# Optimization experiments

Hardware: AMD Instinct MI355X
Metric: run time of the kernel (lower is better)

The kernel has to match this reference:

```python
import jax, jax.numpy as jnp
import numpy as np

N = 8192
D_IN = 256
D_HID = 256
D_OUT = 256


def setup_inputs() -> dict:
    key = jax.random.key(0)
    k_x, k_a, k_q, k_k, k_v = jax.random.split(key, 5)
    X = jax.random.normal(k_x, (N, D_IN), dtype=jnp.float32)
    # binary adjacency, zero diagonal (module adds self-loops via +eye)
    A = jax.random.randint(k_a, (N, N), 0, 2, dtype=jnp.int32)
    A = A * (1 - jnp.eye(N, dtype=jnp.int32))
    # parameters: randn / 10, as in the torch __init__
    Wq = jax.random.normal(k_q, (D_IN, D_HID), dtype=jnp.float32) / 10.0
    Wk = jax.random.normal(k_k, (D_IN, D_HID), dtype=jnp.float32) / 10.0
    Wv = jax.random.normal(k_v, (D_IN, D_OUT), dtype=jnp.float32) / 10.0
    return {"X": X, "A": A, "Wq": Wq, "Wk": Wk, "Wv": Wv}


def reference(X, A, Wq, Wk, Wv):
    n = A.shape[0]
    Af = A.astype(X.dtype) + jnp.eye(n, dtype=X.dtype)  # add self-loops
    Q = X @ Wq  # [N, H]
    K = X @ Wk  # [N, H]
    V = X @ Wv  # [N, O]
    S = Q @ K.T  # [N, N]
    # torch: nan_to_num(-inf*(1-A), nan=0) -> 0 where A==1, finite-min where A==0
    mask = jnp.nan_to_num(-jnp.inf * (1.0 - Af), nan=0.0)
    P = jax.nn.softmax(S + mask, axis=1)
    return P @ V  # [N, O]
```

## Files before the change

kernel.cpp:

```cpp
#include <hip/hip_runtime.h>
#include <stdint.h>


typedef _Float16 f16;
typedef unsigned short u16;
typedef __attribute__((ext_vector_type(8))) _Float16 f16x8;
typedef __attribute__((ext_vector_type(4))) _Float16 f16x4;
typedef __attribute__((ext_vector_type(4))) float f32x4;

#define NN 8192
#define DD 256
#define BR 128
#define BC 64
#define CCH 4
#define COLS (NN / CCH)
#define NIT (COLS / BC)

#define MFMA(a, b, c) __builtin_amdgcn_mfma_f32_16x16x32_f16((a), (b), (c), 0, 0, 0)

__device__ __forceinline__ void gl2lds16(const void* g, void* l) {
    __builtin_amdgcn_global_load_lds(
        (const __attribute__((address_space(1))) unsigned int*)g,
        (__attribute__((address_space(3))) unsigned int*)l, 16, 0, 0);
}

__device__ __forceinline__ u16 f16bits(f16 h) {
    union { f16 h; u16 u; } c;
    c.h = h;
    return c.u;
}

__global__ void splitX_kernel(const float4* __restrict__ X, f16x4* __restrict__ Xh,
                              f16x4* __restrict__ Xl) {
    const int i = blockIdx.x * blockDim.x + threadIdx.x;
    const float4 v = X[i];
    const f16 h0 = (f16)v.x, h1 = (f16)v.y, h2 = (f16)v.z, h3 = (f16)v.w;
    f16x4 H = {h0, h1, h2, h3};
    f16x4 L = {(f16)(v.x - (float)h0), (f16)(v.y - (float)h1), (f16)(v.z - (float)h2),
               (f16)(v.w - (float)h3)};
    Xh[i] = H;
    Xl[i] = L;
}

__global__ void splitW_kernel(const float* __restrict__ Wq, const float* __restrict__ Wk,
                              const float* __restrict__ Wv, f16* __restrict__ WtH,
                              f16* __restrict__ WtL) {
    const int i = blockIdx.x * blockDim.x + threadIdx.x;
    const int mat = i >> 16;
    const int k = (i >> 8) & 255;
    const int n = i & 255;
    const float* W = (mat == 0) ? Wq : ((mat == 1) ? Wk : Wv);
    const float v = W[k * 256 + n];
    const f16 h = (f16)v;
    const size_t o = (size_t)(mat * 256 + n) * 256 + k;
    WtH[o] = h;
    WtL[o] = (f16)(v - (float)h);
}

__global__ __launch_bounds__(256, 2) void qkv_kernel(
    const f16* __restrict__ Xh, const f16* __restrict__ Xl,
    const f16* __restrict__ WtH, const f16* __restrict__ WtL,
    f16* __restrict__ Qh, f16* __restrict__ Ql,
    f16* __restrict__ Kh, f16* __restrict__ Vt) {
    __shared__ f16 Wh[64 * 256];
    __shared__ f16 Wl[64 * 256];
    const int lane = threadIdx.x & 63;
    const int w = threadIdx.x >> 6;
    const int l15 = lane & 15;
    const int quad = lane >> 4;
    const int r0 = blockIdx.x * 64;
    const int mat = blockIdx.y;

    f16x8 xh[8], xl[8];
    const size_t xb = (size_t)(r0 + w * 16 + l15) * DD + quad * 8;
#pragma unroll
    for (int kc = 0; kc < 8; ++kc) {
        xh[kc] = *(const f16x8*)(Xh + xb + kc * 32);
        xl[kc] = *(const f16x8*)(Xl + xb + kc * 32);
    }
    const int orow = r0 + w * 16 + quad * 4;

#pragma unroll 1
    for (int c = 0; c < 4; ++c) {
        const int nb = mat * 256 + c * 64;
#pragma unroll
        for (int i = 0; i < 8; ++i) {
            const int r = w * 16 + i * 2 + (lane >> 5);
            gl2lds16(WtH + (size_t)(nb + r) * DD + (((lane & 31) ^ (r & 7)) * 8),
                     &Wh[(w * 16 + i * 2) * 256]);
        }
#pragma unroll
        for (int i = 0; i < 8; ++i) {
            const int r = w * 16 + i * 2 + (lane >> 5);
            gl2lds16(WtL + (size_t)(nb + r) * DD + (((lane & 31) ^ (r & 7)) * 8),
                     &Wl[(w * 16 + i * 2) * 256]);
        }
        __syncthreads();

        const f32x4 fzero = {0.f, 0.f, 0.f, 0.f};
        f32x4 acc[4];
#pragma unroll
        for (int nt = 0; nt < 4; ++nt) acc[nt] = fzero;
#pragma unroll
        for (int kc = 0; kc < 8; ++kc)
#pragma unroll
            for (int nt = 0; nt < 4; ++nt) {
                const int r = nt * 16 + l15;
                const int blk = (((kc * 4 + quad) ^ (r & 7)) * 8);
                const f16x8 wh = *(const f16x8*)&Wh[r * 256 + blk];
                const f16x8 wl = *(const f16x8*)&Wl[r * 256 + blk];
                acc[nt] = MFMA(xh[kc], wh, acc[nt]);
                acc[nt] = MFMA(xh[kc], wl, acc[nt]);
                acc[nt] = MFMA(xl[kc], wh, acc[nt]);
            }

        if (mat == 0) {
#pragma unroll
            for (int nt = 0; nt < 4; ++nt)
#pragma unroll
                for (int rg = 0; rg < 4; ++rg) {
                    const int col = c * 64 + nt * 16 + l15;
                    const float v = acc[nt][rg];
                    const f16 h = (f16)v;
                    Qh[(size_t)(orow + rg) * DD + col] = h;
                    Ql[(size_t)(orow + rg) * DD + col] = (f16)(v - (float)h);
                }
        } else if (mat == 1) {
#pragma unroll
            for (int nt = 0; nt < 4; ++nt)
#pragma unroll
                for (int rg = 0; rg < 4; ++rg) {
                    const int col = c * 64 + nt * 16 + l15;
                    Kh[(size_t)(orow + rg) * DD + col] = (f16)acc[nt][rg];
                }
        } else {
#pragma unroll
            for (int nt = 0; nt < 4; ++nt) {
                const int n = c * 64 + nt * 16 + l15;
                ushort4 pk;
                pk.x = f16bits((f16)acc[nt][0]);
                pk.y = f16bits((f16)acc[nt][1]);
                pk.z = f16bits((f16)acc[nt][2]);
                pk.w = f16bits((f16)acc[nt][3]);
                *(ushort4*)(Vt + (size_t)n * NN + orow) = pk;
            }
        }
        __syncthreads();
    }
}

__global__ __launch_bounds__(512, 2) void flash_kernel(
    const f16* __restrict__ Qh, const f16* __restrict__ Ql,
    const f16* __restrict__ Kh, const f16* __restrict__ Vt,
    const int* __restrict__ A,
    float* __restrict__ pO, float* __restrict__ pM, float* __restrict__ pL) {
    __shared__ f16 Klds[2][64 * 256];
    __shared__ f16 Vlds[2][256 * 64];
    __shared__ f16 Plds[8][16 * 72];

    const int lane = threadIdx.x & 63;
    const int w = threadIdx.x >> 6;
    const int l15 = lane & 15;
    const int quad = lane >> 4;
    const int bid = blockIdx.x;
    const int cch = bid & 3;
    const int r0 = (bid >> 2) * BR;
    const int col0 = cch * COLS;

    f16x8 qh[8], ql[8];
    {
        const size_t qb = (size_t)(r0 + w * 16 + l15) * DD + quad * 8;
#pragma unroll
        for (int kc = 0; kc < 8; ++kc) {
            qh[kc] = *(const f16x8*)(Qh + qb + kc * 32);
            ql[kc] = *(const f16x8*)(Ql + qb + kc * 32);
        }
    }

    const f32x4 fzero = {0.f, 0.f, 0.f, 0.f};
    f32x4 accO[16];
#pragma unroll
    for (int i = 0; i < 16; ++i) accO[i] = fzero;
    float mrow[4], lrow[4];
#pragma unroll
    for (int r = 0; r < 4; ++r) {
        mrow[r] = -1e30f;
        lrow[r] = 0.f;
    }
    const int growb = r0 + w * 16 + quad * 4;
    f16* Pw = &Plds[w][0];

    auto stage = [&](int t, int b) {
        const int j0 = col0 + t * BC;
#pragma unroll
        for (int i = 0; i < 4; ++i) {
            const int r = w * 8 + i * 2 + (lane >> 5);
            gl2lds16(Kh + (size_t)(j0 + r) * DD + (((lane & 31) ^ (r & 7)) * 8),
                     &Klds[b][(w * 8 + i * 2) * 256]);
        }
#pragma unroll
        for (int i = 0; i < 4; ++i) {
            const int n = w * 32 + i * 8 + (lane >> 3);
            gl2lds16(Vt + (size_t)n * NN + j0 + (((lane & 7) ^ (n & 7)) * 8),
                     &Vlds[b][(w * 32 + i * 8) * 64]);
        }
    };

    stage(0, 0);
    __syncthreads();

#pragma unroll 1
    for (int it = 0; it < NIT; ++it) {
        const int cur = it & 1;
        const int j0 = col0 + it * BC;

        if (it + 1 < NIT) stage(it + 1, cur ^ 1);

        int av[4][4];
#pragma unroll
        for (int rgi = 0; rgi < 4; ++rgi)
#pragma unroll
            for (int jt = 0; jt < 4; ++jt)
                av[rgi][jt] = __builtin_nontemporal_load(
                    A + (size_t)(growb + rgi) * NN + j0 + jt * 16 + l15);

        f32x4 accS[4];
#pragma unroll
        for (int jt = 0; jt < 4; ++jt) accS[jt] = fzero;
#pragma unroll
        for (int kc = 0; kc < 8; ++kc)
#pragma unroll
            for (int jt = 0; jt < 4; ++jt) {
                const int r = jt * 16 + l15;
                const f16x8 kf =
                    *(const f16x8*)&Klds[cur][r * 256 + (((kc * 4 + quad) ^ (r & 7)) * 8)];
                accS[jt] = MFMA(qh[kc], kf, accS[jt]);
                accS[jt] = MFMA(ql[kc], kf, accS[jt]);
            }

        float alpha[4];
#pragma unroll
        for (int rgi = 0; rgi < 4; ++rgi) {
            const int gr = growb + rgi;
            float mx = -3.0e38f;
#pragma unroll
            for (int jt = 0; jt < 4; ++jt) {
                const int gc = j0 + jt * 16 + l15;
                float s = (av[rgi][jt] != 0 || gr == gc) ? accS[jt][rgi] : -3.0e38f;
                accS[jt][rgi] = s;
                mx = fmaxf(mx, s);
            }
#pragma unroll
            for (int off = 1; off < 16; off <<= 1) mx = fmaxf(mx, __shfl_xor(mx, off, 64));
            const float mnew = fmaxf(mrow[rgi], mx);
            alpha[rgi] = __expf(mrow[rgi] - mnew);
            mrow[rgi] = mnew;
            float rs = 0.f;
#pragma unroll
            for (int jt = 0; jt < 4; ++jt) {
                const float s = accS[jt][rgi];
                const float e = (s > -1.0e37f) ? __expf(s - mnew) : 0.f;
                rs += e;
                Pw[(quad * 4 + rgi) * 72 + jt * 16 + l15] = (f16)e;
            }
#pragma unroll
            for (int off = 1; off < 16; off <<= 1) rs += __shfl_xor(rs, off, 64);
            lrow[rgi] = lrow[rgi] * alpha[rgi] + rs;
        }
#pragma unroll
        for (int nt = 0; nt < 16; ++nt)
#pragma unroll
            for (int rgi = 0; rgi < 4; ++rgi) accO[nt][rgi] *= alpha[rgi];

        f16x8 pf[2];
        pf[0] = *(const f16x8*)&Pw[l15 * 72 + quad * 8];
        pf[1] = *(const f16x8*)&Pw[l15 * 72 + 32 + quad * 8];

#pragma unroll
        for (int nt = 0; nt < 16; ++nt)
#pragma unroll
            for (int kc2 = 0; kc2 < 2; ++kc2) {
                const int n = nt * 16 + l15;
                const f16x8 vf =
                    *(const f16x8*)&Vlds[cur][n * 64 + (((kc2 * 4 + quad) ^ (n & 7)) * 8)];
                accO[nt] = MFMA(pf[kc2], vf, accO[nt]);
            }

        __syncthreads();
    }

#pragma unroll
    for (int nt = 0; nt < 16; ++nt)
#pragma unroll
        for (int rgi = 0; rgi < 4; ++rgi)
            pO[((size_t)cch * NN + growb + rgi) * DD + nt * 16 + l15] = accO[nt][rgi];
    if (l15 == 0) {
#pragma unroll
        for (int rgi = 0; rgi < 4; ++rgi) {
            pM[(size_t)cch * NN + growb + rgi] = mrow[rgi];
            pL[(size_t)cch * NN + growb + rgi] = lrow[rgi];
        }
    }
}

__global__ __launch_bounds__(256) void merge_kernel(const float* __restrict__ pO,
                                                    const float* __restrict__ pM,
                                                    const float* __restrict__ pL,
                                                    float* __restrict__ out) {
    const int n = threadIdx.x;
#pragma unroll 1
    for (int rr = 0; rr < 8; ++rr) {
        const int row = blockIdx.x * 8 + rr;
        float mc[CCH], lc[CCH];
        float M = -3e38f;
#pragma unroll
        for (int c = 0; c < CCH; ++c) {
            mc[c] = pM[(size_t)c * NN + row];
            lc[c] = pL[(size_t)c * NN + row];
            M = fmaxf(M, mc[c]);
        }
        float L = 0.f, acc = 0.f;
#pragma unroll
        for (int c = 0; c < CCH; ++c) {
            const float wgt = __expf(mc[c] - M);
            L += wgt * lc[c];
            acc += wgt * pO[((size_t)c * NN + row) * DD + n];
        }
        out[(size_t)row * DD + n] = acc / L;
    }
}

extern "C" void kernel_launch(void* const* d_in, const int* in_sizes, int n_in,
                              void* d_out, int out_size, void* d_ws, size_t ws_size,
                              hipStream_t stream) {
    const float* X = (const float*)d_in[0];
    const int* A = (const int*)d_in[1];
    const float* Wq = (const float*)d_in[2];
    const float* Wk = (const float*)d_in[3];
    const float* Wv = (const float*)d_in[4];
    float* out = (float*)d_out;

    char* ws = (char*)d_ws;
    const size_t MB = 1ull << 20;
    f16* Xh = (f16*)(ws + 0 * MB);
    f16* Xl = (f16*)(ws + 4 * MB);
    f16* WtH = (f16*)(ws + 8 * MB);
    f16* WtL = (f16*)(ws + 8 * MB + 512 * 1024);
    f16* Qh = (f16*)(ws + 9 * MB);
    f16* Ql = (f16*)(ws + 13 * MB);
    f16* Kh = (f16*)(ws + 17 * MB);
    f16* Vt = (f16*)(ws + 21 * MB);
    float* pO = (float*)(ws + 25 * MB);
    float* pM = (float*)(ws + 57 * MB);
    float* pL = (float*)(ws + 57 * MB + 256 * 1024);
    (void)ws_size; (void)in_sizes; (void)n_in; (void)out_size;

    splitX_kernel<<<2048, 256, 0, stream>>>((const float4*)X, (f16x4*)Xh, (f16x4*)Xl);
    splitW_kernel<<<768, 256, 0, stream>>>(Wq, Wk, Wv, WtH, WtL);
    qkv_kernel<<<dim3(NN / 64, 3), 256, 0, stream>>>(Xh, Xl, WtH, WtL, Qh, Ql, Kh, Vt);
    flash_kernel<<<(NN / BR) * CCH, 512, 0, stream>>>(Qh, Ql, Kh, Vt, A, pO, pM, pL);
    merge_kernel<<<NN / 8, 256, 0, stream>>>(pO, pM, pL, out);
}
```

Before: 506.3 us.

## Repartition PV matmul across warps with shared P tile and fp16 max reduction

```diff
diff --git a/kernel.cpp b/kernel.cpp
--- a/kernel.cpp
+++ b/kernel.cpp
@@ -29,6 +29,11 @@
     c.h = h;
     return c.u;
 }
+
+union F16x2U {
+    unsigned u;
+    struct { f16 lo, hi; } f;
+};
 
 __global__ void splitX_kernel(const float4* __restrict__ X, f16x4* __restrict__ Xh,
                               f16x4* __restrict__ Xl) {
@@ -156,7 +161,8 @@
     float* __restrict__ pO, float* __restrict__ pM, float* __restrict__ pL) {
     __shared__ f16 Klds[2][64 * 256];
     __shared__ f16 Vlds[2][256 * 64];
-    __shared__ f16 Plds[8][16 * 72];
+    __shared__ f16 Plds[128 * 64];
+    __shared__ float alds[128];
 
     const int lane = threadIdx.x & 63;
     const int w = threadIdx.x >> 6;
@@ -178,17 +184,20 @@
     }
 
     const f32x4 fzero = {0.f, 0.f, 0.f, 0.f};
-    f32x4 accO[16];
-#pragma unroll
-    for (int i = 0; i < 16; ++i) accO[i] = fzero;
-    float mrow[4], lrow[4];
+    f32x4 accO[2][8];
+#pragma unroll
+    for (int mt = 0; mt < 2; ++mt)
+#pragma unroll
+        for (int nt = 0; nt < 8; ++nt) accO[mt][nt] = fzero;
+    float mrow[4], lpart[4];
 #pragma unroll
     for (int r = 0; r < 4; ++r) {
         mrow[r] = -1e30f;
-        lrow[r] = 0.f;
-    }
-    const int growb = r0 + w * 16 + quad * 4;
-    f16* Pw = &Plds[w][0];
+        lpart[r] = 0.f;
+    }
+    const int srow = r0 + w * 16 + quad * 4;
+    const int prow = (w & 3) * 32;
+    const int pn0 = (w >> 2) * 128;
 
     auto stage = [&](int t, int b) {
         const int j0 = col0 + t * BC;
@@ -222,7 +231,7 @@
 #pragma unroll
             for (int jt = 0; jt < 4; ++jt)
                 av[rgi][jt] = __builtin_nontemporal_load(
-                    A + (size_t)(growb + rgi) * NN + j0 + jt * 16 + l15);
+                    A + (size_t)(srow + rgi) * NN + j0 + jt * 16 + l15);
 
         f32x4 accS[4];
 #pragma unroll
@@ -238,67 +247,119 @@
                 accS[jt] = MFMA(ql[kc], kf, accS[jt]);
             }
 
-        float alpha[4];
+        float mx[4];
 #pragma unroll
         for (int rgi = 0; rgi < 4; ++rgi) {
-            const int gr = growb + rgi;
-            float mx = -3.0e38f;
+            const int gr = srow + rgi;
+            float m = -3.0e38f;
 #pragma unroll
             for (int jt = 0; jt < 4; ++jt) {
                 const int gc = j0 + jt * 16 + l15;
-                float s = (av[rgi][jt] != 0 || gr == gc) ? accS[jt][rgi] : -3.0e38f;
+                const float s = (av[rgi][jt] != 0 || gr == gc) ? accS[jt][rgi] : -3.0e38f;
                 accS[jt][rgi] = s;
-                mx = fmaxf(mx, s);
-            }
-#pragma unroll
-            for (int off = 1; off < 16; off <<= 1) mx = fmaxf(mx, __shfl_xor(mx, off, 64));
-            const float mnew = fmaxf(mrow[rgi], mx);
+                m = fmaxf(m, s);
+            }
+            mx[rgi] = m;
+        }
+        {
+            F16x2U a, b;
+            a.f.lo = (f16)mx[0];
+            a.f.hi = (f16)mx[1];
+            b.f.lo = (f16)mx[2];
+            b.f.hi = (f16)mx[3];
+#pragma unroll
+            for (int off = 1; off < 16; off <<= 1) {
+                F16x2U as, bs;
+                as.u = __shfl_xor(a.u, off, 64);
+                bs.u = __shfl_xor(b.u, off, 64);
+                a.f.lo = (as.f.lo > a.f.lo) ? as.f.lo : a.f.lo;
+                a.f.hi = (as.f.hi > a.f.hi) ? as.f.hi : a.f.hi;
+                b.f.lo = (bs.f.lo > b.f.lo) ? bs.f.lo : b.f.lo;
+                b.f.hi = (bs.f.hi > b.f.hi) ? bs.f.hi : b.f.hi;
+            }
+            mx[0] = (float)a.f.lo;
+            mx[1] = (float)a.f.hi;
+            mx[2] = (float)b.f.lo;
+            mx[3] = (float)b.f.hi;
+        }
+
+        float alpha[4];
+#pragma unroll
+        for (int rgi = 0; rgi < 4; ++rgi) {
+            const float mnew = fmaxf(mrow[rgi], mx[rgi]);
             alpha[rgi] = __expf(mrow[rgi] - mnew);
             mrow[rgi] = mnew;
             float rs = 0.f;
+            const int lrow = w * 16 + quad * 4 + rgi;
 #pragma unroll
             for (int jt = 0; jt < 4; ++jt) {
                 const float s = accS[jt][rgi];
                 const float e = (s > -1.0e37f) ? __expf(s - mnew) : 0.f;
                 rs += e;
-                Pw[(quad * 4 + rgi) * 72 + jt * 16 + l15] = (f16)e;
-            }
-#pragma unroll
-            for (int off = 1; off < 16; off <<= 1) rs += __shfl_xor(rs, off, 64);
-            lrow[rgi] = lrow[rgi] * alpha[rgi] + rs;
-        }
-#pragma unroll
-        for (int nt = 0; nt < 16; ++nt)
-#pragma unroll
-            for (int rgi = 0; rgi < 4; ++rgi) accO[nt][rgi] *= alpha[rgi];
-
-        f16x8 pf[2];
-        pf[0] = *(const f16x8*)&Pw[l15 * 72 + quad * 8];
-        pf[1] = *(const f16x8*)&Pw[l15 * 72 + 32 + quad * 8];
-
-#pragma unroll
-        for (int nt = 0; nt < 16; ++nt)
-#pragma unroll
-            for (int kc2 = 0; kc2 < 2; ++kc2) {
-                const int n = nt * 16 + l15;
+                const int col = jt * 16 + l15;
+                Plds[lrow * 64 + (((col >> 3) ^ (lrow & 7)) * 8) + (col & 7)] = (f16)e;
+            }
+            lpart[rgi] = lpart[rgi] * alpha[rgi] + rs;
+        }
+        if (l15 == 0) *(f32x4*)&alds[w * 16 + quad * 4] = *(f32x4*)alpha;
+        __syncthreads();
+
+        f32x4 alphap[2];
+#pragma unroll
+        for (int mt = 0; mt < 2; ++mt) {
+            alphap[mt] = *(const f32x4*)&alds[prow + mt * 16 + quad * 4];
+#pragma unroll
+            for (int nt = 0; nt < 8; ++nt)
+#pragma unroll
+                for (int rgi = 0; rgi < 4; ++rgi) accO[mt][nt][rgi] *= alphap[mt][rgi];
+        }
+
+        f16x8 pf[2][2];
+#pragma unroll
+        for (int mt = 0; mt < 2; ++mt)
+#pragma unroll
+            for (int kc = 0; kc < 2; ++kc) {
+                const int rr = prow + mt * 16 + l15;
+                pf[mt][kc] =
+                    *(const f16x8*)&Plds[rr * 64 + (((kc * 4 + quad) ^ (rr & 7)) * 8)];
+            }
+
+#pragma unroll
+        for (int nt = 0; nt < 8; ++nt)
+#pragma unroll
+            for (int kc = 0; kc < 2; ++kc) {
+                const int n = pn0 + nt * 16 + l15;
                 const f16x8 vf =
-                    *(const f16x8*)&Vlds[cur][n * 64 + (((kc2 * 4 + quad) ^ (n & 7)) * 8)];
-                accO[nt] = MFMA(pf[kc2], vf, accO[nt]);
+                    *(const f16x8*)&Vlds[cur][n * 64 + (((kc * 4 + quad) ^ (n & 7)) * 8)];
+#pragma unroll
+                for (int mt = 0; mt < 2; ++mt)
+                    accO[mt][nt] = MFMA(pf[mt][kc], vf, accO[mt][nt]);
             }
 
         __syncthreads();
     }
 
 #pragma unroll
-    for (int nt = 0; nt < 16; ++nt)
-#pragma unroll
-        for (int rgi = 0; rgi < 4; ++rgi)
-            pO[((size_t)cch * NN + growb + rgi) * DD + nt * 16 + l15] = accO[nt][rgi];
+    for (int rgi = 0; rgi < 4; ++rgi)
+#pragma unroll
+        for (int off = 1; off < 16; off <<= 1)
+            lpart[rgi] += __shfl_xor(lpart[rgi], off, 64);
+
+#pragma unroll
+    for (int mt = 0; mt < 2; ++mt)
+#pragma unroll
+        for (int nt = 0; nt < 8; ++nt)
+#pragma unroll
+            for (int rgi = 0; rgi < 4; ++rgi) {
+                const int grow = r0 + prow + mt * 16 + quad * 4 + rgi;
+                pO[((size_t)cch * NN + grow) * DD + pn0 + nt * 16 + l15] =
+                    accO[mt][nt][rgi];
+            }
     if (l15 == 0) {
 #pragma unroll
         for (int rgi = 0; rgi < 4; ++rgi) {
-            pM[(size_t)cch * NN + growb + rgi] = mrow[rgi];
-            pL[(size_t)cch * NN + growb + rgi] = lrow[rgi];
+            pM[(size_t)cch * NN + srow + rgi] = mrow[rgi];
+            pL[(size_t)cch * NN + srow + rgi] = lpart[rgi];
         }
     }
 }
```

After: 513.3 us. No clear change (+1.4%).
